# Kernel tuning notes

Measured on AMD Instinct MI355X. Metric: run time of the kernel, lower is better.

## Reference

```python
import jax, jax.numpy as jnp
import numpy as np

N, E, DIM = 50000, 1_600_000, 96
H = DIM // 3      # num_heads = dim/3 = 32
HD = 3            # head_dim = dim/num_heads = 3
SCALE = 2.0
EPS = 1e-5


def ln(x, g, b):
    mu = x.mean(-1, keepdims=True)
    var = ((x - mu) ** 2).mean(-1, keepdims=True)
    return (x - mu) * jax.lax.rsqrt(var + EPS) * g + b


def setup_inputs() -> dict:
    key = jax.random.key(0)
    ks = jax.random.split(key, 40)
    rn = lambda k, shp, s=0.05: jax.random.normal(k, shp, jnp.float32) * s
    inp = {
        'feat': jax.random.normal(ks[0], (N, DIM), jnp.float32),
        'edge': jax.random.normal(ks[1], (E, H), jnp.float32),
        'Wq': rn(ks[2], (DIM, DIM)), 'bq': jnp.zeros((DIM,), jnp.float32),
        'Wk': rn(ks[3], (DIM, DIM)), 'bk': jnp.zeros((DIM,), jnp.float32),
        'Wv': rn(ks[4], (DIM, DIM)), 'bv': jnp.zeros((DIM,), jnp.float32),
        'We': rn(ks[5], (H, H)), 'be': jnp.zeros((H,), jnp.float32),
        'Wb': rn(ks[6], (H, H)), 'bb': jnp.zeros((H,), jnp.float32),
        'Wvv': rn(ks[7], (DIM + H, DIM)), 'bvv': jnp.zeros((DIM,), jnp.float32),
        'Wf0': rn(ks[8], (H, 2 * H)), 'bf0': jnp.zeros((2 * H,), jnp.float32),
        'Wf1': rn(ks[9], (2 * H, H)), 'bf1': jnp.zeros((H,), jnp.float32),
        'Wm0': rn(ks[10], (DIM, 2 * DIM)), 'bm0': jnp.zeros((2 * DIM,), jnp.float32),
        'Wm1': rn(ks[11], (2 * DIM, DIM)), 'bm1': jnp.zeros((DIM,), jnp.float32),
        'g_n0': jnp.ones((DIM,), jnp.float32), 'b_n0': jnp.zeros((DIM,), jnp.float32),
        'g_e0': jnp.ones((H,), jnp.float32), 'b_e0': jnp.zeros((H,), jnp.float32),
        'g_e1': jnp.ones((H,), jnp.float32), 'b_e1': jnp.zeros((H,), jnp.float32),
        'g_m': jnp.ones((DIM,), jnp.float32), 'b_m': jnp.zeros((DIM,), jnp.float32),
        'w': jnp.zeros((1,), jnp.float32),
        'src': jax.random.randint(ks[12], (E,), 0, N),
        'dst': jax.random.randint(ks[13], (E,), 0, N),
    }
    return inp


def reference(feat, edge, Wq, bq, Wk, bk, Wv, bv, We, be, Wb, bb, Wvv, bvv,
              Wf0, bf0, Wf1, bf1, Wm0, bm0, Wm1, bm1,
              g_n0, b_n0, g_e0, b_e0, g_e1, b_e1, g_m, b_m, w, src, dst):
    n = feat.shape[0]
    h0 = ln(feat, g_n0, b_n0)            # [N, DIM]
    ew = ln(edge, g_e0, b_e0)            # [E, H]
    q = (h0 @ Wq + bq).reshape(n, H, HD)
    k = (h0 @ Wk + bk).reshape(n, H, HD)
    v = (h0 @ Wv + bv).reshape(n, H, HD)
    ve = (ew @ We + be)[:, :, None]       # [E, H, 1]
    B = ew @ Wb + bb                      # [E, H]
    # src_dot_dst('k','q'): (k[src] * q[dst]).sum(-1)
    score = jnp.sum(k[src] * q[dst], axis=-1) / SCALE + B   # [E, H]
    e = score + edge                       # [E, H]
    se = jnp.concatenate([v[src], ve], axis=-1)              # [E, H, 4]
    # edge_softmax: softmax over incoming edges of each dst node, per head
    m = jax.ops.segment_max(score, dst, num_segments=n)      # [N, H]
    ex = jnp.exp(score - m[dst])
    den = jax.ops.segment_sum(ex, dst, num_segments=n)
    att = (ex / den[dst])[:, :, None]                        # [E, H, 1]
    agg = jax.ops.segment_sum(att * se, dst, num_segments=n) # [N, H, 4]
    h = feat * (1.0 + w) + (agg.reshape(n, -1) @ Wvv + bvv)  # [N, DIM]
    # up_expert Mlp (pre-LN residual)
    hn = ln(h, g_m, b_m)
    h = h + (jax.nn.relu(hn @ Wm0 + bm0) @ Wm1 + bm1)
    # edge FFN residual
    en = ln(e, g_e1, b_e1)
    e = e + (jax.nn.relu(en @ Wf0 + bf0) @ Wf1 + bf1)
    return h, e
```

## Files before the change

### kernel.cpp

```cpp
#include <hip/hip_runtime.h>
#include <cstdint>
#include <cstddef>


typedef short  s16x8 __attribute__((ext_vector_type(8)));
typedef short  s16x4 __attribute__((ext_vector_type(4)));
typedef float  f32x4 __attribute__((ext_vector_type(4)));

__device__ __forceinline__ unsigned short f2b(float x) {
    union { float f; unsigned u; } v; v.f = x;
    unsigned r = v.u + 0x7FFF + ((v.u >> 16) & 1);
    return (unsigned short)(r >> 16);
}
__device__ __forceinline__ float b2f(unsigned short u) {
    union { unsigned u; float f; } v; v.u = ((unsigned)u) << 16; return v.f;
}

template<int MULTI, int LNA, int A16, int RELU, int RES>
__global__ __launch_bounds__(256) void mgemm_kernel(
    const void* __restrict__ Av, int lda,
    const float* __restrict__ B0, const float* __restrict__ B1,
    const float* __restrict__ B2, int ldb,
    const float* __restrict__ bias0, const float* __restrict__ bias1,
    const float* __restrict__ bias2,
    const float* __restrict__ lng, const float* __restrict__ lnbv,
    const float* __restrict__ resid, const float* __restrict__ wptr,
    float* __restrict__ C, int ldc, unsigned short* __restrict__ C16,
    int M, int K)
{
    __shared__ unsigned short sAL[64 * 200];
    __shared__ unsigned short sB[96 * 40];

    const int tid = threadIdx.x;
    const int m0 = blockIdx.x * 64;
    const int y  = blockIdx.y;
    const float* B = MULTI ? (y == 0 ? B0 : (y == 1 ? B1 : B2)) : B0;
    const int nbB = MULTI ? 0 : y * 96;
    const int nbC = y * 96;
    const int w = tid >> 6, l = tid & 63, fr = l & 15, kg = l >> 4;
    const int KP = K + 8;

    if (LNA) {
        const float* Af = (const float*)Av;
        const int row = 16 * w + fr;
        const int grow = m0 + row;
        float x[24];
        if (grow < M) {
            #pragma unroll
            for (int t = 0; t < 6; t++)
                *(float4*)&x[t * 4] = *(const float4*)(Af + (size_t)grow * lda + 24 * kg + t * 4);
        } else {
            #pragma unroll
            for (int t = 0; t < 24; t++) x[t] = 0.f;
        }
        float s = 0.f;
        #pragma unroll
        for (int t = 0; t < 24; t++) s += x[t];
        s += __shfl_xor(s, 16, 64); s += __shfl_xor(s, 32, 64);
        float mu = s * (1.f / 96.f);
        float v2 = 0.f;
        #pragma unroll
        for (int t = 0; t < 24; t++) { float d = x[t] - mu; v2 += d * d; }
        v2 += __shfl_xor(v2, 16, 64); v2 += __shfl_xor(v2, 32, 64);
        float rs = rsqrtf(v2 * (1.f / 96.f) + 1e-5f);
        #pragma unroll
        for (int t3 = 0; t3 < 3; t3++) {
            s16x8 yv;
            #pragma unroll
            for (int u = 0; u < 8; u++) {
                int cidx = 24 * kg + t3 * 8 + u;
                yv[u] = (short)f2b((x[t3 * 8 + u] - mu) * rs * lng[cidx] + lnbv[cidx]);
            }
            *(s16x8*)&sAL[row * KP + 24 * kg + t3 * 8] = yv;
        }
    } else {
        const int nseg = K >> 3;
        for (int idx = tid; idx < 64 * nseg; idx += 256) {
            int row = idx / nseg, k8 = (idx - row * nseg) * 8;
            int grow = m0 + row;
            s16x8 a8 = (s16x8){0, 0, 0, 0, 0, 0, 0, 0};
            if (grow < M) {
                if (A16) {
                    a8 = *(const s16x8*)((const unsigned short*)Av + (size_t)grow * lda + k8);
                } else {
                    const float* Af = (const float*)Av;
                    float4 v0 = *(const float4*)(Af + (size_t)grow * lda + k8);
                    float4 v1 = *(const float4*)(Af + (size_t)grow * lda + k8 + 4);
                    a8[0] = (short)f2b(v0.x); a8[1] = (short)f2b(v0.y);
                    a8[2] = (short)f2b(v0.z); a8[3] = (short)f2b(v0.w);
                    a8[4] = (short)f2b(v1.x); a8[5] = (short)f2b(v1.y);
                    a8[6] = (short)f2b(v1.z); a8[7] = (short)f2b(v1.w);
                }
            }
            *(s16x8*)&sAL[row * KP + k8] = a8;
        }
    }

    f32x4 acc[6];
    #pragma unroll
    for (int i = 0; i < 6; i++) acc[i] = (f32x4){0.f, 0.f, 0.f, 0.f};

    for (int kc = 0; kc < K; kc += 32) {
        #pragma unroll
        for (int r = 0; r < 3; r++) {
            int idx = tid + 256 * r;
            int k = idx / 24, n4 = (idx - k * 24) * 4;
            float4 v = *(const float4*)(B + (size_t)(kc + k) * ldb + nbB + n4);
            sB[(n4 + 0) * 40 + k] = f2b(v.x);
            sB[(n4 + 1) * 40 + k] = f2b(v.y);
            sB[(n4 + 2) * 40 + k] = f2b(v.z);
            sB[(n4 + 3) * 40 + k] = f2b(v.w);
        }
        __syncthreads();
        {
            s16x8 a = *(s16x8*)&sAL[(16 * w + fr) * KP + kc + kg * 8];
            #pragma unroll
            for (int nt = 0; nt < 6; nt++) {
                s16x8 b = *(s16x8*)&sB[(16 * nt + fr) * 40 + kg * 8];
                acc[nt] = __builtin_amdgcn_mfma_f32_16x16x32_bf16(a, b, acc[nt], 0, 0, 0);
            }
        }
        __syncthreads();
    }

    const float* biasp = MULTI ? (y == 0 ? bias0 : (y == 1 ? bias1 : bias2)) : bias0;
    const int bbase = MULTI ? 0 : nbB;

    #pragma unroll
    for (int nt = 0; nt < 6; nt++) {
        int cl = nt * 16 + fr;
        float bv = biasp[bbase + cl];
        int gcol = nbC + cl;
        #pragma unroll
        for (int r = 0; r < 4; r++) {
            int row = m0 + 16 * w + 4 * kg + r;
            if (row >= M) continue;
            float v = acc[nt][r] + bv;
            if (RELU) v = fmaxf(v, 0.f);
            if (MULTI) {
                C16[(size_t)row * 288 + gcol] = f2b(v);
            } else {
                C[(size_t)row * ldc + gcol] = v;
            }
        }
    }
}

__global__ __launch_bounds__(256) void prep_kernel(
    const float* __restrict__ Wb, const float* __restrict__ We,
    const float* __restrict__ Wf0, const float* __restrict__ Wf1,
    const float* __restrict__ Wvv, const float* __restrict__ Wm0,
    const float* __restrict__ Wm1,
    unsigned short* __restrict__ WbWe16, unsigned short* __restrict__ Wf0T16,
    unsigned short* __restrict__ Wf1T16, unsigned short* __restrict__ WvvT16,
    unsigned short* __restrict__ Wm0T16, unsigned short* __restrict__ Wm1T16)
{
    const int t = threadIdx.x;
    for (int i = t; i < 2048; i += 256) {
        int n = i >> 5, k = i & 31;
        float v = (n < 32) ? Wb[k * 32 + n] : We[k * 32 + (n - 32)];
        WbWe16[i] = f2b(v);
    }
    for (int i = t; i < 2048; i += 256) {
        int n = i >> 5, k = i & 31;
        Wf0T16[i] = f2b(Wf0[k * 64 + n]);
    }
    for (int i = t; i < 2048; i += 256) {
        int n = i >> 6, k = i & 63;
        Wf1T16[i] = f2b(Wf1[k * 32 + n]);
    }
    for (int i = t; i < 12288; i += 256) {
        int n = i >> 7, k = i & 127;
        WvvT16[i] = f2b(Wvv[k * 96 + n]);
    }
    for (int i = t; i < 18432; i += 256) {
        int n = i / 96, k = i - n * 96;
        Wm0T16[i] = f2b(Wm0[k * 192 + n]);
    }
    for (int i = t; i < 18432; i += 256) {
        int n = i / 192, k = i - n * 192;
        Wm1T16[i] = f2b(Wm1[k * 96 + n]);
    }
}

__global__ __launch_bounds__(256) void count_kernel(
    const int* __restrict__ dst, int* __restrict__ cnt,
    int* __restrict__ rank, int E)
{
    int i = blockIdx.x * 256 + threadIdx.x;
    if (i < E) rank[i] = atomicAdd(&cnt[dst[i]], 1);
}

__global__ __launch_bounds__(1024) void scan_kernel(
    const int* __restrict__ cnt, int* __restrict__ off, int N)
{
    __shared__ int s[1024];
    const int tid = threadIdx.x;
    const int chunk = (N + 1023) >> 10;
    const int lo = tid * chunk;
    const int hi = min(lo + chunk, N);
    int sum = 0;
    for (int i = lo; i < hi; i++) sum += cnt[i];
    s[tid] = sum;
    __syncthreads();
    for (int d = 1; d < 1024; d <<= 1) {
        int v = (tid >= d) ? s[tid - d] : 0;
        __syncthreads();
        s[tid] += v;
        __syncthreads();
    }
    int base = (tid == 0) ? 0 : s[tid - 1];
    for (int i = lo; i < hi; i++) {
        off[i] = base;
        base += cnt[i];
    }
}

__global__ __launch_bounds__(256) void scatter_kernel(
    const int* __restrict__ dst, const int* __restrict__ src,
    const int* __restrict__ off, const int* __restrict__ rank,
    int4* __restrict__ slotinfo, int E)
{
    int i = blockIdx.x * 256 + threadIdx.x;
    if (i < E) {
        int d = dst[i];
        int p = off[d] + rank[i];
        slotinfo[p] = make_int4(i, src[i], d, 0);
    }
}

__global__ __launch_bounds__(256, 5) void edge_tile_kernel(
    const float* __restrict__ edge, const unsigned short* __restrict__ qkv16,
    const int4* __restrict__ slotinfo,
    const unsigned short* __restrict__ WbWe16,
    const unsigned short* __restrict__ Wf0T16,
    const unsigned short* __restrict__ Wf1T16,
    const float* __restrict__ be, const float* __restrict__ bb,
    const float* __restrict__ bf0, const float* __restrict__ bf1,
    const float* __restrict__ ge0, const float* __restrict__ be0,
    const float* __restrict__ ge1, const float* __restrict__ be1,
    unsigned short* __restrict__ exve16, float* __restrict__ eout, int E)
{
    __shared__ float          sEV[64 * 36];
    __shared__ unsigned short sQK[64 * 44];
    __shared__ unsigned short sA [64 * 40];
    __shared__ unsigned short sX [64 * 76];

    const int tid = threadIdx.x;
    const long long e0 = (long long)blockIdx.x * 64;
    const int w  = tid >> 6;
    const int l  = tid & 63;
    const int fr = l & 15;
    const int kg = l >> 4;

    {
        const int row = tid >> 2;
        const int j   = tid & 3;
        long long s = e0 + row;
        float qv[24], kv[24];
        if (s < E) {
            int4 si = slotinfo[s];
            const unsigned short* qp = qkv16 + (size_t)si.z * 288 + 24 * j;
            const unsigned short* kp = qkv16 + (size_t)si.y * 288 + 96 + 24 * j;
            #pragma unroll
            for (int t = 0; t < 3; t++) {
                s16x8 qa = *(const s16x8*)(qp + 8 * t);
                s16x8 ka = *(const s16x8*)(kp + 8 * t);
                #pragma unroll
                for (int u = 0; u < 8; u++) {
                    qv[8 * t + u] = b2f((unsigned short)qa[u]);
                    kv[8 * t + u] = b2f((unsigned short)ka[u]);
                }
            }
        } else {
            #pragma unroll
            for (int t = 0; t < 24; t++) { qv[t] = 0.f; kv[t] = 0.f; }
        }
        s16x8 qkb;
        #pragma unroll
        for (int t = 0; t < 8; t++) {
            float d = kv[3*t]*qv[3*t] + kv[3*t+1]*qv[3*t+1] + kv[3*t+2]*qv[3*t+2];
            qkb[t] = (short)f2b(0.5f * d);
        }
        *(s16x8*)&sQK[row * 44 + 8 * j] = qkb;
    }
    #pragma unroll
    for (int rr = 0; rr < 2; rr++) {
        int idx = tid + 256 * rr;
        int row = idx >> 3, c4 = (idx & 7) * 4;
        long long s = e0 + row;
        float4 v = make_float4(0.f, 0.f, 0.f, 0.f);
        if (s < E) {
            int ge = slotinfo[s].x;
            v = *(const float4*)(edge + (size_t)ge * 32 + c4);
        }
        *(float4*)&sEV[row * 36 + c4] = v;
    }
    __syncthreads();

    {
        const int row = 16 * w + (tid & 15);
        const int q = (tid & 63) >> 4;
        float x[8];
        *(float4*)&x[0] = *(float4*)&sEV[row * 36 + 8 * q];
        *(float4*)&x[4] = *(float4*)&sEV[row * 36 + 8 * q + 4];
        float s = x[0] + x[1] + x[2] + x[3] + x[4] + x[5] + x[6] + x[7];
        s += __shfl_xor(s, 16, 64); s += __shfl_xor(s, 32, 64);
        float mu = s * (1.f / 32.f);
        float v2 = 0.f;
        #pragma unroll
        for (int i = 0; i < 8; i++) { float d = x[i] - mu; v2 += d * d; }
        v2 += __shfl_xor(v2, 16, 64); v2 += __shfl_xor(v2, 32, 64);
        float rs = rsqrtf(v2 * (1.f / 32.f) + 1e-5f);
        float4 g1 = *(const float4*)(ge0 + 8 * q), g2 = *(const float4*)(ge0 + 8 * q + 4);
        float4 b1 = *(const float4*)(be0 + 8 * q), b2 = *(const float4*)(be0 + 8 * q + 4);
        float gg[8] = {g1.x, g1.y, g1.z, g1.w, g2.x, g2.y, g2.z, g2.w};
        float bs[8] = {b1.x, b1.y, b1.z, b1.w, b2.x, b2.y, b2.z, b2.w};
        s16x8 y;
        #pragma unroll
        for (int i = 0; i < 8; i++)
            y[i] = (short)f2b((x[i] - mu) * rs * gg[i] + bs[i]);
        *(s16x8*)&sA[row * 40 + 8 * q] = y;
    }
    __builtin_amdgcn_wave_barrier();

    f32x4 acc[4];
    {
        s16x8 a = *(s16x8*)&sA[(16 * w + fr) * 40 + kg * 8];
        #pragma unroll
        for (int nt = 0; nt < 4; nt++) {
            s16x8 b = *(const s16x8*)(WbWe16 + (16 * nt + fr) * 32 + kg * 8);
            f32x4 z = {0.f, 0.f, 0.f, 0.f};
            acc[nt] = __builtin_amdgcn_mfma_f32_16x16x32_bf16(a, b, z, 0, 0, 0);
        }
    }

    #pragma unroll
    for (int nt = 0; nt < 2; nt++) {
        int col = nt * 16 + fr;
        float bbv = bb[col];
        #pragma unroll
        for (int r = 0; r < 4; r++) {
            int row = 16 * w + 4 * kg + r;
            float sc = acc[nt][r] + b2f(sQK[row * 44 + col]) + bbv;
            sX[row * 76 + col] = f2b(__expf(sc));
            float er = sc + sEV[row * 36 + col];
            sEV[row * 36 + col] = er;
        }
    }
    #pragma unroll
    for (int nt = 2; nt < 4; nt++) {
        int col = (nt - 2) * 16 + fr;
        float bev = be[col];
        #pragma unroll
        for (int r = 0; r < 4; r++) {
            int row = 16 * w + 4 * kg + r;
            sX[row * 76 + 32 + col] = f2b(acc[nt][r] + bev);
        }
    }
    __syncthreads();

    #pragma unroll
    for (int rr = 0; rr < 2; rr++) {
        int idx = tid + 256 * rr;
        int row = idx >> 3, c8 = (idx & 7) * 8;
        long long s = e0 + row;
        if (s < E)
            *(s16x8*)(exve16 + (size_t)s * 64 + c8) = *(s16x8*)&sX[row * 76 + c8];
    }
    {
        const int row = 16 * w + (tid & 15);
        const int q = (tid & 63) >> 4;
        float x[8];
        *(float4*)&x[0] = *(float4*)&sEV[row * 36 + 8 * q];
        *(float4*)&x[4] = *(float4*)&sEV[row * 36 + 8 * q + 4];
        float s = x[0] + x[1] + x[2] + x[3] + x[4] + x[5] + x[6] + x[7];
        s += __shfl_xor(s, 16, 64); s += __shfl_xor(s, 32, 64);
        float mu = s * (1.f / 32.f);
        float v2 = 0.f;
        #pragma unroll
        for (int i = 0; i < 8; i++) { float d = x[i] - mu; v2 += d * d; }
        v2 += __shfl_xor(v2, 16, 64); v2 += __shfl_xor(v2, 32, 64);
        float rs = rsqrtf(v2 * (1.f / 32.f) + 1e-5f);
        float4 g1 = *(const float4*)(ge1 + 8 * q), g2 = *(const float4*)(ge1 + 8 * q + 4);
        float4 b1 = *(const float4*)(be1 + 8 * q), b2 = *(const float4*)(be1 + 8 * q + 4);
        float gg[8] = {g1.x, g1.y, g1.z, g1.w, g2.x, g2.y, g2.z, g2.w};
        float bs[8] = {b1.x, b1.y, b1.z, b1.w, b2.x, b2.y, b2.z, b2.w};
        s16x8 y;
        #pragma unroll
        for (int i = 0; i < 8; i++)
            y[i] = (short)f2b((x[i] - mu) * rs * gg[i] + bs[i]);
        *(s16x8*)&sA[row * 40 + 8 * q] = y;
    }
    __syncthreads();

    {
        s16x8 a = *(s16x8*)&sA[(16 * w + fr) * 40 + kg * 8];
        #pragma unroll
        for (int nt = 0; nt < 4; nt++) {
            s16x8 b = *(const s16x8*)(Wf0T16 + (16 * nt + fr) * 32 + kg * 8);
            f32x4 z = {0.f, 0.f, 0.f, 0.f};
            f32x4 a2 = __builtin_amdgcn_mfma_f32_16x16x32_bf16(a, b, z, 0, 0, 0);
            int col = nt * 16 + fr;
            float b0v = bf0[col];
            #pragma unroll
            for (int r = 0; r < 4; r++) {
                int row = 16 * w + 4 * kg + r;
                sX[row * 76 + col] = f2b(fmaxf(a2[r] + b0v, 0.f));
            }
        }
    }
    __builtin_amdgcn_wave_barrier();

    {
        s16x8 a0 = *(s16x8*)&sX[(16 * w + fr) * 76 + kg * 8];
        s16x8 a1 = *(s16x8*)&sX[(16 * w + fr) * 76 + 32 + kg * 8];
        #pragma unroll
        for (int nt = 0; nt < 2; nt++) {
            s16x8 b0 = *(const s16x8*)(Wf1T16 + (16 * nt + fr) * 64 + kg * 8);
            s16x8 b1 = *(const s16x8*)(Wf1T16 + (16 * nt + fr) * 64 + 32 + kg * 8);
            f32x4 z = {0.f, 0.f, 0.f, 0.f};
            f32x4 t = __builtin_amdgcn_mfma_f32_16x16x32_bf16(a0, b0, z, 0, 0, 0);
            t = __builtin_amdgcn_mfma_f32_16x16x32_bf16(a1, b1, t, 0, 0, 0);
            int col = nt * 16 + fr;
            float bf1v = bf1[col];
            #pragma unroll
            for (int r = 0; r < 4; r++) {
                int row = 16 * w + 4 * kg + r;
                float out = t[r] + sEV[row * 36 + col] + bf1v;
                sEV[row * 36 + col] = out;
            }
        }
    }
    __syncthreads();

    #pragma unroll
    for (int rr = 0; rr < 2; rr++) {
        int idx = tid + 256 * rr;
        int row = idx >> 3, c4 = (idx & 7) * 4;
        long long s = e0 + row;
        if (s < E) {
            int ge = slotinfo[s].x;
            *(float4*)(eout + (size_t)ge * 32 + c4) = *(float4*)&sEV[row * 36 + c4];
        }
    }
}

__global__ __launch_bounds__(256) void gather_kernel(
    const unsigned short* __restrict__ exve16, const unsigned short* __restrict__ qkv16,
    const int4* __restrict__ slotinfo, const int* __restrict__ off,
    const int* __restrict__ cnt, unsigned short* __restrict__ agg16, int N)
{
    __shared__ unsigned short sV16[4][2][2][96];
    __shared__ unsigned short sE16[4][2][2][64];
    const int wave = threadIdx.x >> 6;
    const int lane = threadIdx.x & 63;
    const int head = lane & 31;
    const int half = lane >> 5;
    int n = blockIdx.x * 4 + wave;
    if (n >= N) return;
    const int o = off[n], d = cnt[n];
    float a0 = 0.f, a1 = 0.f, a2 = 0.f, a3 = 0.f, den = 0.f;
    for (int i = half; i < d; i += 4) {
        const int i2 = i + 2;
        {
            int sn = slotinfo[o + i].y;
            const unsigned short* vr = qkv16 + (size_t)sn * 288 + 192;
            const unsigned short* er = exve16 + (size_t)(o + i) * 64;
            if (head < 12)
                *(s16x8*)&sV16[wave][half][0][head * 8] = *(const s16x8*)(vr + head * 8);
            else if (head >= 24)
                *(s16x8*)&sE16[wave][half][0][(head - 24) * 8] = *(const s16x8*)(er + (head - 24) * 8);
        }
        if (i2 < d) {
            int sn = slotinfo[o + i2].y;
            const unsigned short* vr = qkv16 + (size_t)sn * 288 + 192;
            const unsigned short* er = exve16 + (size_t)(o + i2) * 64;
            if (head < 12)
                *(s16x8*)&sV16[wave][half][1][head * 8] = *(const s16x8*)(vr + head * 8);
            else if (head >= 24)
                *(s16x8*)&sE16[wave][half][1][(head - 24) * 8] = *(const s16x8*)(er + (head - 24) * 8);
        }
        __builtin_amdgcn_wave_barrier();
        {
            float ex = b2f(sE16[wave][half][0][head]);
            float vv = b2f(sE16[wave][half][0][32 + head]);
            a0 += ex * b2f(sV16[wave][half][0][head * 3]);
            a1 += ex * b2f(sV16[wave][half][0][head * 3 + 1]);
            a2 += ex * b2f(sV16[wave][half][0][head * 3 + 2]);
            a3 += ex * vv;
            den += ex;
        }
        if (i2 < d) {
            float ex = b2f(sE16[wave][half][1][head]);
            float vv = b2f(sE16[wave][half][1][32 + head]);
            a0 += ex * b2f(sV16[wave][half][1][head * 3]);
            a1 += ex * b2f(sV16[wave][half][1][head * 3 + 1]);
            a2 += ex * b2f(sV16[wave][half][1][head * 3 + 2]);
            a3 += ex * vv;
            den += ex;
        }
        __builtin_amdgcn_wave_barrier();
    }
    a0 += __shfl_xor(a0, 32, 64);
    a1 += __shfl_xor(a1, 32, 64);
    a2 += __shfl_xor(a2, 32, 64);
    a3 += __shfl_xor(a3, 32, 64);
    den += __shfl_xor(den, 32, 64);
    if (half == 0) {
        float sc = (d > 0) ? 1.f / den : 0.f;
        s16x4 ov;
        ov[0] = (short)f2b(a0 * sc);
        ov[1] = (short)f2b(a1 * sc);
        ov[2] = (short)f2b(a2 * sc);
        ov[3] = (short)f2b(a3 * sc);
        *(s16x4*)(agg16 + (size_t)n * 128 + head * 4) = ov;
    }
}

__global__ __launch_bounds__(256, 2) void mlp_kernel(
    const unsigned short* __restrict__ agg16, const float* __restrict__ feat,
    const unsigned short* __restrict__ WvvT16,
    const unsigned short* __restrict__ Wm0T16,
    const unsigned short* __restrict__ Wm1T16,
    const float* __restrict__ bvv, const float* __restrict__ bm0,
    const float* __restrict__ bm1,
    const float* __restrict__ g_m, const float* __restrict__ b_m,
    const float* __restrict__ wsc,
    float* __restrict__ hout, int M)
{
    __shared__ unsigned short sU[64 * 200];
    __shared__ float          sHP[64 * 100];
    __shared__ unsigned short sA[64 * 104];

    const int tid = threadIdx.x;
    const int m0 = blockIdx.x * 64;
    const int w = tid >> 6, l = tid & 63, fr = l & 15, kg = l >> 4;

    #pragma unroll
    for (int r = 0; r < 4; r++) {
        int s1 = tid + 256 * r;
        int row = s1 >> 4, k8 = (s1 & 15) * 8;
        int grow = m0 + row;
        s16x8 a8 = (s16x8){0, 0, 0, 0, 0, 0, 0, 0};
        if (grow < M) a8 = *(const s16x8*)(agg16 + (size_t)grow * 128 + k8);
        *(s16x8*)&sU[row * 136 + k8] = a8;
    }
    __syncthreads();
    const float w0 = 1.f + wsc[0];

    {
        f32x4 acc[6];
        #pragma unroll
        for (int i = 0; i < 6; i++) acc[i] = (f32x4){0.f, 0.f, 0.f, 0.f};
        #pragma unroll
        for (int kc = 0; kc < 128; kc += 32) {
            s16x8 a = *(s16x8*)&sU[(16 * w + fr) * 136 + kc + kg * 8];
            #pragma unroll
            for (int nt = 0; nt < 6; nt++) {
                s16x8 b = *(const s16x8*)(WvvT16 + (16 * nt + fr) * 128 + kc + kg * 8);
                acc[nt] = __builtin_amdgcn_mfma_f32_16x16x32_bf16(a, b, acc[nt], 0, 0, 0);
            }
        }
        #pragma unroll
        for (int nt = 0; nt < 6; nt++) {
            int col = nt * 16 + fr;
            float bv = bvv[col];
            #pragma unroll
            for (int r = 0; r < 4; r++) {
                int row = 16 * w + 4 * kg + r;
                int grow = m0 + row;
                float fv = (grow < M) ? feat[(size_t)grow * 96 + col] : 0.f;
                sHP[row * 100 + col] = acc[nt][r] + bv + w0 * fv;
            }
        }
    }
    __syncthreads();

    {
        const int row = 16 * w + (tid & 15);
        const int q = (tid & 63) >> 4;
        float x[24];
        #pragma unroll
        for (int t = 0; t < 6; t++)
            *(float4*)&x[t * 4] = *(float4*)&sHP[row * 100 + 24 * q + t * 4];
        float s = 0.f;
        #pragma unroll
        for (int t = 0; t < 24; t++) s += x[t];
        s += __shfl_xor(s, 16, 64); s += __shfl_xor(s, 32, 64);
        float mu = s * (1.f / 96.f);
        float v2 = 0.f;
        #pragma unroll
        for (int t = 0; t < 24; t++) { float d = x[t] - mu; v2 += d * d; }
        v2 += __shfl_xor(v2, 16, 64); v2 += __shfl_xor(v2, 32, 64);
        float rs = rsqrtf(v2 * (1.f / 96.f) + 1e-5f);
        #pragma unroll
        for (int t3 = 0; t3 < 3; t3++) {
            s16x8 yv;
            #pragma unroll
            for (int u = 0; u < 8; u++) {
                int cidx = 24 * q + t3 * 8 + u;
                yv[u] = (short)f2b((x[t3 * 8 + u] - mu) * rs * g_m[cidx] + b_m[cidx]);
            }
            *(s16x8*)&sA[row * 104 + 24 * q + t3 * 8] = yv;
        }
    }
    __builtin_amdgcn_wave_barrier();

    {
        f32x4 acc2[12];
        #pragma unroll
        for (int i = 0; i < 12; i++) acc2[i] = (f32x4){0.f, 0.f, 0.f, 0.f};
        #pragma unroll
        for (int kc = 0; kc < 96; kc += 32) {
            s16x8 a = *(s16x8*)&sA[(16 * w + fr) * 104 + kc + kg * 8];
            #pragma unroll
            for (int nt = 0; nt < 12; nt++) {
                s16x8 b = *(const s16x8*)(Wm0T16 + (16 * nt + fr) * 96 + kc + kg * 8);
                acc2[nt] = __builtin_amdgcn_mfma_f32_16x16x32_bf16(a, b, acc2[nt], 0, 0, 0);
            }
        }
        #pragma unroll
        for (int nt = 0; nt < 12; nt++) {
            int col = nt * 16 + fr;
            float b0 = bm0[col];
            #pragma unroll
            for (int r = 0; r < 4; r++) {
                int row = 16 * w + 4 * kg + r;
                sU[row * 200 + col] = f2b(fmaxf(acc2[nt][r] + b0, 0.f));
            }
        }
    }
    __builtin_amdgcn_wave_barrier();

    {
        f32x4 acc3[6];
        #pragma unroll
        for (int i = 0; i < 6; i++) acc3[i] = (f32x4){0.f, 0.f, 0.f, 0.f};
        #pragma unroll
        for (int kc = 0; kc < 192; kc += 32) {
            s16x8 a = *(s16x8*)&sU[(16 * w + fr) * 200 + kc + kg * 8];
            #pragma unroll
            for (int nt = 0; nt < 6; nt++) {
                s16x8 b = *(const s16x8*)(Wm1T16 + (16 * nt + fr) * 192 + kc + kg * 8);
                acc3[nt] = __builtin_amdgcn_mfma_f32_16x16x32_bf16(a, b, acc3[nt], 0, 0, 0);
            }
        }
        #pragma unroll
        for (int nt = 0; nt < 6; nt++) {
            int col = nt * 16 + fr;
            float bv = bm1[col];
            #pragma unroll
            for (int r = 0; r < 4; r++) {
                int row = 16 * w + 4 * kg + r;
                int grow = m0 + row;
                if (grow < M)
                    hout[(size_t)grow * 96 + col] = acc3[nt][r] + bv + sHP[row * 100 + col];
            }
        }
    }
}

extern "C" void kernel_launch(void* const* d_in, const int* in_sizes, int n_in,
                              void* d_out, int out_size, void* d_ws, size_t ws_size,
                              hipStream_t stream)
{
    (void)n_in; (void)out_size; (void)ws_size;
    const float* feat = (const float*)d_in[0];
    const float* edge = (const float*)d_in[1];
    const float* Wq   = (const float*)d_in[2];
    const float* bq   = (const float*)d_in[3];
    const float* Wk   = (const float*)d_in[4];
    const float* bk   = (const float*)d_in[5];
    const float* Wv   = (const float*)d_in[6];
    const float* bv   = (const float*)d_in[7];
    const float* We   = (const float*)d_in[8];
    const float* be   = (const float*)d_in[9];
    const float* Wb   = (const float*)d_in[10];
    const float* bb   = (const float*)d_in[11];
    const float* Wvv  = (const float*)d_in[12];
    const float* bvv  = (const float*)d_in[13];
    const float* Wf0  = (const float*)d_in[14];
    const float* bf0  = (const float*)d_in[15];
    const float* Wf1  = (const float*)d_in[16];
    const float* bf1  = (const float*)d_in[17];
    const float* Wm0  = (const float*)d_in[18];
    const float* bm0  = (const float*)d_in[19];
    const float* Wm1  = (const float*)d_in[20];
    const float* bm1  = (const float*)d_in[21];
    const float* g_n0 = (const float*)d_in[22];
    const float* b_n0 = (const float*)d_in[23];
    const float* g_e0 = (const float*)d_in[24];
    const float* b_e0 = (const float*)d_in[25];
    const float* g_e1 = (const float*)d_in[26];
    const float* b_e1 = (const float*)d_in[27];
    const float* g_m  = (const float*)d_in[28];
    const float* b_m  = (const float*)d_in[29];
    const float* wsc  = (const float*)d_in[30];
    const int*   src  = (const int*)d_in[31];
    const int*   dst  = (const int*)d_in[32];

    const int N = in_sizes[0] / 96;
    const int E = in_sizes[1] / 32;

    unsigned short* agg16 = (unsigned short*)d_ws;
    unsigned short* qkv16 = agg16 + (size_t)N * 128;
    unsigned short* exve16 = qkv16 + (size_t)N * 288;
    unsigned short* wbwe16 = exve16 + (size_t)E * 64;
    unsigned short* wf0t16 = wbwe16 + 2048;
    unsigned short* wf1t16 = wf0t16 + 2048;
    unsigned short* wvvt16 = wf1t16 + 2048;
    unsigned short* wm0t16 = wvvt16 + 12288;
    unsigned short* wm1t16 = wm0t16 + 18432;
    int4*  slotinfo = (int4*)(((uintptr_t)(wm1t16 + 18432) + 15) & ~(uintptr_t)15);
    int*   rank  = (int*)(slotinfo + E);
    int*   cnt   = rank + E;
    int*   offv  = cnt + N;
    float* hout  = (float*)d_out;
    float* eoutp = (float*)d_out + (size_t)N * 96;

    hipMemsetAsync(cnt, 0, (size_t)N * sizeof(int), stream);

    const int mt = (N + 63) / 64;
    const int et = (E + 255) / 256;

    prep_kernel<<<1, 256, 0, stream>>>(Wb, We, Wf0, Wf1, Wvv, Wm0, Wm1,
                                       wbwe16, wf0t16, wf1t16, wvvt16, wm0t16, wm1t16);
    count_kernel<<<et, 256, 0, stream>>>(dst, cnt, rank, E);
    scan_kernel<<<1, 1024, 0, stream>>>(cnt, offv, N);
    scatter_kernel<<<et, 256, 0, stream>>>(dst, src, offv, rank, slotinfo, E);

    mgemm_kernel<1,1,0,0,0><<<dim3(mt, 3), 256, 0, stream>>>(
        feat, 96, Wq, Wk, Wv, 96, bq, bk, bv, g_n0, b_n0,
        nullptr, nullptr, nullptr, 0, qkv16, N, 96);

    edge_tile_kernel<<<(E + 63) / 64, 256, 0, stream>>>(edge, qkv16, slotinfo,
                                             wbwe16, wf0t16, wf1t16,
                                             be, bb, bf0, bf1,
                                             g_e0, b_e0, g_e1, b_e1,
                                             exve16, eoutp, E);

    gather_kernel<<<(N + 3) / 4, 256, 0, stream>>>(exve16, qkv16, slotinfo, offv, cnt, agg16, N);

    mlp_kernel<<<mt, 256, 0, stream>>>(agg16, feat, wvvt16, wm0t16, wm1t16,
                                       bvv, bm0, bm1, g_m, b_m, wsc, hout, N);
}
```

Before: 795.1 us.

## Shrink shared buffers to bf16, raise occupancy, deepen gather batching

The edge kernel now keeps its edge and residual tile in bf16 shared memory instead of fp32 and raises its occupancy hint from 5 to 6 blocks. It also writes the edge output straight from the MFMA fragments with scattered scalar stores, dropping the staged coalesced float4 write and a barrier. The aggregation kernel gathers 4 edges per half-wave per iteration instead of 2, for more loads in flight. The MLP kernel stores its residual tile in bf16 and raises its occupancy hint to 3, which cuts LDS use but lowers residual and edge-output precision to bf16.

```diff
diff --git a/kernel.cpp b/kernel.cpp
--- a/kernel.cpp
+++ b/kernel.cpp
@@ -229,7 +229,7 @@
     }
 }
 
-__global__ __launch_bounds__(256, 5) void edge_tile_kernel(
+__global__ __launch_bounds__(256, 6) void edge_tile_kernel(
     const float* __restrict__ edge, const unsigned short* __restrict__ qkv16,
     const int4* __restrict__ slotinfo,
     const unsigned short* __restrict__ WbWe16,
@@ -241,7 +241,7 @@
     const float* __restrict__ ge1, const float* __restrict__ be1,
     unsigned short* __restrict__ exve16, float* __restrict__ eout, int E)
 {
-    __shared__ float          sEV[64 * 36];
+    __shared__ unsigned short sEV[64 * 40];
     __shared__ unsigned short sQK[64 * 44];
     __shared__ unsigned short sA [64 * 40];
     __shared__ unsigned short sX [64 * 76];
@@ -294,16 +294,19 @@
             int ge = slotinfo[s].x;
             v = *(const float4*)(edge + (size_t)ge * 32 + c4);
         }
-        *(float4*)&sEV[row * 36 + c4] = v;
+        s16x4 vb; vb[0] = (short)f2b(v.x); vb[1] = (short)f2b(v.y);
+        vb[2] = (short)f2b(v.z); vb[3] = (short)f2b(v.w);
+        *(s16x4*)&sEV[row * 40 + c4] = vb;
     }
     __syncthreads();
 
     {
         const int row = 16 * w + (tid & 15);
         const int q = (tid & 63) >> 4;
+        s16x8 xa = *(s16x8*)&sEV[row * 40 + 8 * q];
         float x[8];
-        *(float4*)&x[0] = *(float4*)&sEV[row * 36 + 8 * q];
-        *(float4*)&x[4] = *(float4*)&sEV[row * 36 + 8 * q + 4];
+        #pragma unroll
+        for (int u = 0; u < 8; u++) x[u] = b2f((unsigned short)xa[u]);
         float s = x[0] + x[1] + x[2] + x[3] + x[4] + x[5] + x[6] + x[7];
         s += __shfl_xor(s, 16, 64); s += __shfl_xor(s, 32, 64);
         float mu = s * (1.f / 32.f);
@@ -344,8 +347,8 @@
             int row = 16 * w + 4 * kg + r;
             float sc = acc[nt][r] + b2f(sQK[row * 44 + col]) + bbv;
             sX[row * 76 + col] = f2b(__expf(sc));
-            float er = sc + sEV[row * 36 + col];
-            sEV[row * 36 + col] = er;
+            float er = sc + b2f(sEV[row * 40 + col]);
+            sEV[row * 40 + col] = f2b(er);
         }
     }
     #pragma unroll
@@ -371,9 +374,10 @@
     {
         const int row = 16 * w + (tid & 15);
         const int q = (tid & 63) >> 4;
+        s16x8 xa = *(s16x8*)&sEV[row * 40 + 8 * q];
         float x[8];
-        *(float4*)&x[0] = *(float4*)&sEV[row * 36 + 8 * q];
-        *(float4*)&x[4] = *(float4*)&sEV[row * 36 + 8 * q + 4];
+        #pragma unroll
+        for (int u = 0; u < 8; u++) x[u] = b2f((unsigned short)xa[u]);
         float s = x[0] + x[1] + x[2] + x[3] + x[4] + x[5] + x[6] + x[7];
         s += __shfl_xor(s, 16, 64); s += __shfl_xor(s, 32, 64);
         float mu = s * (1.f / 32.f);
@@ -427,21 +431,13 @@
             #pragma unroll
             for (int r = 0; r < 4; r++) {
                 int row = 16 * w + 4 * kg + r;
-                float out = t[r] + sEV[row * 36 + col] + bf1v;
-                sEV[row * 36 + col] = out;
-            }
-        }
-    }
-    __syncthreads();
-
-    #pragma unroll
-    for (int rr = 0; rr < 2; rr++) {
-        int idx = tid + 256 * rr;
-        int row = idx >> 3, c4 = (idx & 7) * 4;
-        long long s = e0 + row;
-        if (s < E) {
-            int ge = slotinfo[s].x;
-            *(float4*)(eout + (size_t)ge * 32 + c4) = *(float4*)&sEV[row * 36 + c4];
+                long long s = e0 + row;
+                if (s < E) {
+                    int ge = slotinfo[s].x;
+                    eout[(size_t)ge * 32 + col] =
+                        t[r] + b2f(sEV[row * 40 + col]) + bf1v;
+                }
+            }
         }
     }
 }
@@ -451,8 +447,8 @@
     const int4* __restrict__ slotinfo, const int* __restrict__ off,
     const int* __restrict__ cnt, unsigned short* __restrict__ agg16, int N)
 {
-    __shared__ unsigned short sV16[4][2][2][96];
-    __shared__ unsigned short sE16[4][2][2][64];
+    __shared__ unsigned short sV16[4][2][4][96];
+    __shared__ unsigned short sE16[4][2][4][64];
     const int wave = threadIdx.x >> 6;
     const int lane = threadIdx.x & 63;
     const int head = lane & 31;
@@ -461,44 +457,33 @@
     if (n >= N) return;
     const int o = off[n], d = cnt[n];
     float a0 = 0.f, a1 = 0.f, a2 = 0.f, a3 = 0.f, den = 0.f;
-    for (int i = half; i < d; i += 4) {
-        const int i2 = i + 2;
-        {
-            int sn = slotinfo[o + i].y;
-            const unsigned short* vr = qkv16 + (size_t)sn * 288 + 192;
-            const unsigned short* er = exve16 + (size_t)(o + i) * 64;
-            if (head < 12)
-                *(s16x8*)&sV16[wave][half][0][head * 8] = *(const s16x8*)(vr + head * 8);
-            else if (head >= 24)
-                *(s16x8*)&sE16[wave][half][0][(head - 24) * 8] = *(const s16x8*)(er + (head - 24) * 8);
-        }
-        if (i2 < d) {
-            int sn = slotinfo[o + i2].y;
-            const unsigned short* vr = qkv16 + (size_t)sn * 288 + 192;
-            const unsigned short* er = exve16 + (size_t)(o + i2) * 64;
-            if (head < 12)
-                *(s16x8*)&sV16[wave][half][1][head * 8] = *(const s16x8*)(vr + head * 8);
-            else if (head >= 24)
-                *(s16x8*)&sE16[wave][half][1][(head - 24) * 8] = *(const s16x8*)(er + (head - 24) * 8);
+    for (int i = half; i < d; i += 8) {
+        #pragma unroll
+        for (int b = 0; b < 4; b++) {
+            int ii = i + 2 * b;
+            if (ii < d) {
+                int sn = slotinfo[o + ii].y;
+                const unsigned short* vr = qkv16 + (size_t)sn * 288 + 192;
+                const unsigned short* er = exve16 + (size_t)(o + ii) * 64;
+                if (head < 12)
+                    *(s16x8*)&sV16[wave][half][b][head * 8] = *(const s16x8*)(vr + head * 8);
+                else if (head >= 24)
+                    *(s16x8*)&sE16[wave][half][b][(head - 24) * 8] = *(const s16x8*)(er + (head - 24) * 8);
+            }
         }
         __builtin_amdgcn_wave_barrier();
-        {
-            float ex = b2f(sE16[wave][half][0][head]);
-            float vv = b2f(sE16[wave][half][0][32 + head]);
-            a0 += ex * b2f(sV16[wave][half][0][head * 3]);
-            a1 += ex * b2f(sV16[wave][half][0][head * 3 + 1]);
-            a2 += ex * b2f(sV16[wave][half][0][head * 3 + 2]);
-            a3 += ex * vv;
-            den += ex;
-        }
-        if (i2 < d) {
-            float ex = b2f(sE16[wave][half][1][head]);
-            float vv = b2f(sE16[wave][half][1][32 + head]);
-            a0 += ex * b2f(sV16[wave][half][1][head * 3]);
-            a1 += ex * b2f(sV16[wave][half][1][head * 3 + 1]);
-            a2 += ex * b2f(sV16[wave][half][1][head * 3 + 2]);
-            a3 += ex * vv;
-            den += ex;
+        #pragma unroll
+        for (int b = 0; b < 4; b++) {
+            int ii = i + 2 * b;
+            if (ii < d) {
+                float ex = b2f(sE16[wave][half][b][head]);
+                float vv = b2f(sE16[wave][half][b][32 + head]);
+                a0 += ex * b2f(sV16[wave][half][b][head * 3]);
+                a1 += ex * b2f(sV16[wave][half][b][head * 3 + 1]);
+                a2 += ex * b2f(sV16[wave][half][b][head * 3 + 2]);
+                a3 += ex * vv;
+                den += ex;
+            }
         }
         __builtin_amdgcn_wave_barrier();
     }
@@ -518,7 +503,7 @@
     }
 }
 
-__global__ __launch_bounds__(256, 2) void mlp_kernel(
+__global__ __launch_bounds__(256, 3) void mlp_kernel(
     const unsigned short* __restrict__ agg16, const float* __restrict__ feat,
     const unsigned short* __restrict__ WvvT16,
     const unsigned short* __restrict__ Wm0T16,
@@ -530,7 +515,7 @@
     float* __restrict__ hout, int M)
 {
     __shared__ unsigned short sU[64 * 200];
-    __shared__ float          sHP[64 * 100];
+    __shared__ unsigned short sHP[64 * 104];
     __shared__ unsigned short sA[64 * 104];
 
     const int tid = threadIdx.x;
@@ -571,7 +556,7 @@
                 int row = 16 * w + 4 * kg + r;
                 int grow = m0 + row;
                 float fv = (grow < M) ? feat[(size_t)grow * 96 + col] : 0.f;
-                sHP[row * 100 + col] = acc[nt][r] + bv + w0 * fv;
+                sHP[row * 104 + col] = f2b(acc[nt][r] + bv + w0 * fv);
             }
         }
     }
@@ -582,8 +567,11 @@
         const int q = (tid & 63) >> 4;
         float x[24];
         #pragma unroll
-        for (int t = 0; t < 6; t++)
-            *(float4*)&x[t * 4] = *(float4*)&sHP[row * 100 + 24 * q + t * 4];
+        for (int t = 0; t < 3; t++) {
+            s16x8 xa = *(s16x8*)&sHP[row * 104 + 24 * q + 8 * t];
+            #pragma unroll
+            for (int u = 0; u < 8; u++) x[8 * t + u] = b2f((unsigned short)xa[u]);
+        }
         float s = 0.f;
         #pragma unroll
         for (int t = 0; t < 24; t++) s += x[t];
@@ -655,7 +643,8 @@
                 int row = 16 * w + 4 * kg + r;
                 int grow = m0 + row;
                 if (grow < M)
-                    hout[(size_t)grow * 96 + col] = acc3[nt][r] + bv + sHP[row * 100 + col];
+                    hout[(size_t)grow * 96 + col] =
+                        acc3[nt][r] + bv + b2f(sHP[row * 104 + col]);
             }
         }
     }
```

Measured after the change: 821.9 us. +3.4%, slower.
